# Performance work log

Hardware: AMD Instinct MI355X
Metric: run time of the kernel (lower is better)

Reference implementation:

```python
import jax, jax.numpy as jnp
import numpy as np
from jax.ops import segment_sum, segment_max

IN_CH, HID, OUT_CH, HEADS = 128, 64, 32, 4
N_NODES, N_EDGES = 50000, 800000
NEG_SLOPE = 0.2
EPS = 1e-16


def gat_layer(x, edge_index, W, att_src, att_dst, bias, heads, out_ch, concat):
    """PyG-style GATConv (add_self_loops=False, dropout=0, no edge features)."""
    N = x.shape[0]
    src, dst = edge_index[0], edge_index[1]
    h = (x @ W).reshape(N, heads, out_ch)                 # [N, H, C]
    a_src = jnp.einsum('nhc,hc->nh', h, att_src)          # [N, H]
    a_dst = jnp.einsum('nhc,hc->nh', h, att_dst)          # [N, H]
    e = jax.nn.leaky_relu(a_src[src] + a_dst[dst], NEG_SLOPE)  # [E, H]
    # segment softmax over incoming edges of each dst node
    m = segment_max(e, dst, num_segments=N)               # [N, H]
    ex = jnp.exp(e - m[dst])                              # [E, H]
    s = segment_sum(ex, dst, num_segments=N)              # [N, H]
    alpha = ex / (s[dst] + EPS)                           # [E, H]
    msg = h[src] * alpha[..., None]                       # [E, H, C]
    out = segment_sum(msg, dst, num_segments=N)           # [N, H, C]
    if concat:
        out = out.reshape(N, heads * out_ch)
    else:
        out = out.mean(axis=1)
    return out + bias, alpha


def setup_inputs() -> dict:
    key = jax.random.key(0)
    ks = jax.random.split(key, 10)
    s_in = 1.0 / np.sqrt(IN_CH)
    s_h = 1.0 / np.sqrt(HEADS * HID)
    return {
        'x': jax.random.normal(ks[0], (N_NODES, IN_CH), jnp.float32),
        'edge_index': jax.random.randint(ks[1], (2, N_EDGES), 0, N_NODES, jnp.int32),
        'W1': jax.random.normal(ks[2], (IN_CH, HEADS * HID), jnp.float32) * s_in,
        'att_src1': jax.random.normal(ks[3], (HEADS, HID), jnp.float32) * s_h,
        'att_dst1': jax.random.normal(ks[4], (HEADS, HID), jnp.float32) * s_h,
        'bias1': jnp.zeros((HEADS * HID,), jnp.float32),
        'W2': jax.random.normal(ks[5], (HEADS * HID, OUT_CH), jnp.float32) * s_h,
        'att_src2': jax.random.normal(ks[6], (1, OUT_CH), jnp.float32) * s_h,
        'att_dst2': jax.random.normal(ks[7], (1, OUT_CH), jnp.float32) * s_h,
        'bias2': jnp.zeros((OUT_CH,), jnp.float32),
    }


def reference(x, edge_index, W1, att_src1, att_dst1, bias1, W2, att_src2, att_dst2, bias2):
    h1, alpha1 = gat_layer(x, edge_index, W1, att_src1, att_dst1, bias1, HEADS, HID, concat=True)
    h1 = jax.nn.elu(h1)
    h2, alpha2 = gat_layer(h1, edge_index, W2, att_src2, att_dst2, bias2, 1, OUT_CH, concat=False)
    return h2, edge_index, alpha1, edge_index, alpha2
```

## Files before the change

### kernel.cpp

```cpp
#include <hip/hip_runtime.h>
#include <hip/hip_fp16.h>
#include <math.h>

#define NEG_SLOPE 0.2f
#define EPS_C 1e-16f

typedef _Float16 f16x8 __attribute__((ext_vector_type(8)));
typedef float f32x4 __attribute__((ext_vector_type(4)));

__device__ __forceinline__ float lrelu(float x){ return x > 0.f ? x : NEG_SLOPE * x; }
__device__ __forceinline__ float eluf(float x){ return x > 0.f ? x : expm1f(x); }

__global__ void zero_int_kernel(int* __restrict__ p, int n){
  int i = blockIdx.x * blockDim.x + threadIdx.x;
  if (i < n) p[i] = 0;
}

__global__ void count_deg_kernel(const int* __restrict__ dst, int* __restrict__ deg, int E){
  int i = blockIdx.x * blockDim.x + threadIdx.x;
  if (i < E) atomicAdd(&deg[dst[i]], 1);
}

__global__ __launch_bounds__(256) void scan1_kernel(const int* __restrict__ deg,
    int* __restrict__ offsets, int* __restrict__ blockSums, int N){
  __shared__ int sm[256];
  int b = blockIdx.x, t = threadIdx.x;
  int i = b * 256 + t;
  int v = (i < N) ? deg[i] : 0;
  sm[t] = v;
  __syncthreads();
  #pragma unroll
  for (int st = 1; st < 256; st <<= 1){
    int add = (t >= st) ? sm[t - st] : 0;
    __syncthreads();
    sm[t] += add;
    __syncthreads();
  }
  if (i < N) offsets[i] = sm[t] - v;
  if (t == 255) blockSums[b] = sm[255];
}

__global__ __launch_bounds__(256) void scan2_kernel(const int* __restrict__ blockSums,
    int* __restrict__ blockBase, int* __restrict__ offsetsN, int nb){
  __shared__ int sm[256];
  int t = threadIdx.x;
  int v = (t < nb) ? blockSums[t] : 0;
  sm[t] = v;
  __syncthreads();
  #pragma unroll
  for (int st = 1; st < 256; st <<= 1){
    int add = (t >= st) ? sm[t - st] : 0;
    __syncthreads();
    sm[t] += add;
    __syncthreads();
  }
  if (t < nb) blockBase[t] = sm[t] - v;
  if (t == 255) *offsetsN = sm[255];
}

__global__ __launch_bounds__(256) void scan3_kernel(int* __restrict__ offsets,
    const int* __restrict__ blockBase, int* __restrict__ cursor, int N){
  int b = blockIdx.x, t = threadIdx.x;
  int i = b * 256 + t;
  if (i < N){
    int v = offsets[i] + blockBase[b];
    offsets[i] = v;
    cursor[i] = v;
  }
}

__global__ void scatter_kernel(const int* __restrict__ src, const int* __restrict__ dst,
                               int* __restrict__ cursor, int* __restrict__ csr_src,
                               int* __restrict__ csr_eid, int E){
  int i = blockIdx.x * blockDim.x + threadIdx.x;
  if (i < E){
    int d = dst[i];
    int p = atomicAdd(&cursor[d], 1);
    csr_src[p] = src[i];
    csr_eid[p] = i;
  }
}

__global__ void cvt_x_kernel(const float* __restrict__ x, __half* __restrict__ x16, int n4){
  int i = blockIdx.x * blockDim.x + threadIdx.x;
  if (i < n4){
    float4 v = *reinterpret_cast<const float4*>(&x[(size_t)i * 4]);
    __half2 h01 = __floats2half2_rn(v.x, v.y);
    __half2 h23 = __floats2half2_rn(v.z, v.w);
    uint2 pack;
    pack.x = *reinterpret_cast<unsigned int*>(&h01);
    pack.y = *reinterpret_cast<unsigned int*>(&h23);
    *reinterpret_cast<uint2*>(&x16[(size_t)i * 4]) = pack;
  }
}

__global__ void cvt_w1_kernel(const float* __restrict__ W1, __half* __restrict__ W1t){
  int i = blockIdx.x * blockDim.x + threadIdx.x;
  int k = i >> 8, c = i & 255;
  if (i < 128 * 256) W1t[(size_t)c * 128 + k] = __float2half(W1[(size_t)k * 256 + c]);
}

__global__ void cvt_w2_kernel(const float* __restrict__ W2, __half* __restrict__ W2t){
  int i = blockIdx.x * blockDim.x + threadIdx.x;
  int k = i >> 5, c = i & 31;
  if (i < 256 * 32) W2t[(size_t)c * 256 + k] = __float2half(W2[(size_t)k * 32 + c]);
}

__global__ __launch_bounds__(256) void gemm1_kernel(const __half* __restrict__ x16,
    const __half* __restrict__ W1t, const float* __restrict__ att_src,
    const float* __restrict__ att_dst, __half* __restrict__ h1,
    float* __restrict__ a_src_f, float* __restrict__ a_dst_f, int N){
  __shared__ _Float16 As[128 * 136];
  __shared__ _Float16 Bs[64 * 136];
  int tid = threadIdx.x;
  int lane = tid & 63, wid = tid >> 6;
  int rowBase = blockIdx.x * 128;
  int head = blockIdx.y;
  int colBase = head * 64;

  #pragma unroll
  for (int it = 0; it < 8; ++it){
    int li = it * 256 + tid;
    int r = li >> 4, seg = li & 15;
    int grow = rowBase + r;
    f16x8 v = {};
    if (grow < N) v = *reinterpret_cast<const f16x8*>(&x16[(size_t)grow * 128 + seg * 8]);
    *reinterpret_cast<f16x8*>(&As[r * 136 + seg * 8]) = v;
  }
  #pragma unroll
  for (int it = 0; it < 4; ++it){
    int li = it * 256 + tid;
    int c = li >> 4, seg = li & 15;
    f16x8 v = *reinterpret_cast<const f16x8*>(&W1t[(size_t)(colBase + c) * 128 + seg * 8]);
    *reinterpret_cast<f16x8*>(&Bs[c * 136 + seg * 8]) = v;
  }
  __syncthreads();

  f32x4 acc[2][4] = {};
  int l15 = lane & 15, l4 = lane >> 4;
  #pragma unroll
  for (int ks = 0; ks < 4; ++ks){
    int kOff = ks * 32 + l4 * 8;
    f16x8 a0 = *reinterpret_cast<const f16x8*>(&As[(wid * 32 + l15) * 136 + kOff]);
    f16x8 a1 = *reinterpret_cast<const f16x8*>(&As[(wid * 32 + 16 + l15) * 136 + kOff]);
    #pragma unroll
    for (int cc = 0; cc < 4; ++cc){
      f16x8 b = *reinterpret_cast<const f16x8*>(&Bs[(cc * 16 + l15) * 136 + kOff]);
      acc[0][cc] = __builtin_amdgcn_mfma_f32_16x16x32_f16(a0, b, acc[0][cc], 0, 0, 0);
      acc[1][cc] = __builtin_amdgcn_mfma_f32_16x16x32_f16(a1, b, acc[1][cc], 0, 0, 0);
    }
  }

  #pragma unroll
  for (int rr = 0; rr < 2; ++rr){
    #pragma unroll
    for (int i = 0; i < 4; ++i){
      int row = rowBase + wid * 32 + rr * 16 + l4 * 4 + i;
      if (row < N){
        #pragma unroll
        for (int cc = 0; cc < 4; ++cc)
          h1[(size_t)row * 256 + colBase + cc * 16 + l15] = __float2half(acc[rr][cc][i]);
      }
    }
  }
  float sw[4], dw[4];
  #pragma unroll
  for (int cc = 0; cc < 4; ++cc){
    sw[cc] = att_src[colBase + cc * 16 + l15];
    dw[cc] = att_dst[colBase + cc * 16 + l15];
  }
  #pragma unroll
  for (int rr = 0; rr < 2; ++rr){
    #pragma unroll
    for (int i = 0; i < 4; ++i){
      float ts = 0.f, td = 0.f;
      #pragma unroll
      for (int cc = 0; cc < 4; ++cc){
        ts += acc[rr][cc][i] * sw[cc];
        td += acc[rr][cc][i] * dw[cc];
      }
      #pragma unroll
      for (int st = 8; st > 0; st >>= 1){
        ts += __shfl_xor(ts, st);
        td += __shfl_xor(td, st);
      }
      int row = rowBase + wid * 32 + rr * 16 + l4 * 4 + i;
      if (l15 == 0 && row < N){
        a_src_f[(size_t)row * 4 + head] = ts;
        a_dst_f[(size_t)row * 4 + head] = td;
      }
    }
  }
}

__global__ __launch_bounds__(256) void node1_kernel(
    const __half* __restrict__ h1, const float4* __restrict__ a_src,
    const float* __restrict__ a_src_f, const float4* __restrict__ a_dst,
    const int* __restrict__ offsets, const int* __restrict__ csr_src,
    const int* __restrict__ csr_eid, const float* __restrict__ bias,
    __half* __restrict__ h1b, float* __restrict__ alpha1_out, int N){
  __shared__ float al_lds[4][4][64];
  int gid = blockIdx.x * blockDim.x + threadIdx.x;
  int n = gid >> 6, lane = gid & 63, wid = (threadIdx.x >> 6) & 3;
  if (n >= N) return;
  int off = offsets[n];
  int deg = offsets[n + 1] - off;
  float4 ad = a_dst[n];
  bool have0 = (lane < deg);
  float4 e0 = make_float4(-INFINITY, -INFINITY, -INFINITY, -INFINITY);
  if (have0){
    float4 as = a_src[csr_src[off + lane]];
    e0 = make_float4(lrelu(as.x + ad.x), lrelu(as.y + ad.y),
                     lrelu(as.z + ad.z), lrelu(as.w + ad.w));
  }
  float m0 = e0.x, m1 = e0.y, m2 = e0.z, m3 = e0.w;
  for (int i = lane + 64; i < deg; i += 64){
    float4 as = a_src[csr_src[off + i]];
    m0 = fmaxf(m0, lrelu(as.x + ad.x));
    m1 = fmaxf(m1, lrelu(as.y + ad.y));
    m2 = fmaxf(m2, lrelu(as.z + ad.z));
    m3 = fmaxf(m3, lrelu(as.w + ad.w));
  }
  #pragma unroll
  for (int st = 32; st > 0; st >>= 1){
    m0 = fmaxf(m0, __shfl_xor(m0, st));
    m1 = fmaxf(m1, __shfl_xor(m1, st));
    m2 = fmaxf(m2, __shfl_xor(m2, st));
    m3 = fmaxf(m3, __shfl_xor(m3, st));
  }
  float s0 = 0.f, s1 = 0.f, s2 = 0.f, s3 = 0.f;
  if (have0){
    s0 = __expf(e0.x - m0); s1 = __expf(e0.y - m1);
    s2 = __expf(e0.z - m2); s3 = __expf(e0.w - m3);
  }
  for (int i = lane + 64; i < deg; i += 64){
    float4 as = a_src[csr_src[off + i]];
    s0 += __expf(lrelu(as.x + ad.x) - m0);
    s1 += __expf(lrelu(as.y + ad.y) - m1);
    s2 += __expf(lrelu(as.z + ad.z) - m2);
    s3 += __expf(lrelu(as.w + ad.w) - m3);
  }
  #pragma unroll
  for (int st = 32; st > 0; st >>= 1){
    s0 += __shfl_xor(s0, st); s1 += __shfl_xor(s1, st);
    s2 += __shfl_xor(s2, st); s3 += __shfl_xor(s3, st);
  }
  float i0 = 1.f / (s0 + EPS_C), i1 = 1.f / (s1 + EPS_C);
  float i2 = 1.f / (s2 + EPS_C), i3 = 1.f / (s3 + EPS_C);
  if (have0){
    float a0 = __expf(e0.x - m0) * i0, a1 = __expf(e0.y - m1) * i1;
    float a2 = __expf(e0.z - m2) * i2, a3 = __expf(e0.w - m3) * i3;
    al_lds[wid][0][lane] = a0; al_lds[wid][1][lane] = a1;
    al_lds[wid][2][lane] = a2; al_lds[wid][3][lane] = a3;
    int eid = csr_eid[off + lane];
    *reinterpret_cast<float4*>(&alpha1_out[(size_t)eid * 4]) = make_float4(a0, a1, a2, a3);
  }
  for (int i = lane + 64; i < deg; i += 64){
    int slot = off + i;
    float4 as = a_src[csr_src[slot]];
    int eid = csr_eid[slot];
    *reinterpret_cast<float4*>(&alpha1_out[(size_t)eid * 4]) =
        make_float4(__expf(lrelu(as.x + ad.x) - m0) * i0,
                    __expf(lrelu(as.y + ad.y) - m1) * i1,
                    __expf(lrelu(as.z + ad.z) - m2) * i2,
                    __expf(lrelu(as.w + ad.w) - m3) * i3);
  }
  int head = lane >> 4;
  float mh  = head == 0 ? m0 : head == 1 ? m1 : head == 2 ? m2 : m3;
  float ih  = head == 0 ? i0 : head == 1 ? i1 : head == 2 ? i2 : i3;
  float adh = head == 0 ? ad.x : head == 1 ? ad.y : head == 2 ? ad.z : ad.w;
  float4 accA = make_float4(0.f, 0.f, 0.f, 0.f);
  float4 accB = make_float4(0.f, 0.f, 0.f, 0.f);
  float4 accC = make_float4(0.f, 0.f, 0.f, 0.f);
  float4 accD = make_float4(0.f, 0.f, 0.f, 0.f);
  int degL = deg < 64 ? deg : 64;
  int j = 0;
  for (; j + 3 < degL; j += 4){
    int sA = csr_src[off + j];
    int sB = csr_src[off + j + 1];
    int sC = csr_src[off + j + 2];
    int sD = csr_src[off + j + 3];
    float alA = al_lds[wid][head][j];
    float alB = al_lds[wid][head][j + 1];
    float alC = al_lds[wid][head][j + 2];
    float alD = al_lds[wid][head][j + 3];
    float2 rA = *reinterpret_cast<const float2*>(&h1[(size_t)sA * 256 + lane * 4]);
    float2 rB = *reinterpret_cast<const float2*>(&h1[(size_t)sB * 256 + lane * 4]);
    float2 rC = *reinterpret_cast<const float2*>(&h1[(size_t)sC * 256 + lane * 4]);
    float2 rD = *reinterpret_cast<const float2*>(&h1[(size_t)sD * 256 + lane * 4]);
    float2 fA0 = __half22float2(*reinterpret_cast<__half2*>(&rA.x));
    float2 fA1 = __half22float2(*reinterpret_cast<__half2*>(&rA.y));
    float2 fB0 = __half22float2(*reinterpret_cast<__half2*>(&rB.x));
    float2 fB1 = __half22float2(*reinterpret_cast<__half2*>(&rB.y));
    float2 fC0 = __half22float2(*reinterpret_cast<__half2*>(&rC.x));
    float2 fC1 = __half22float2(*reinterpret_cast<__half2*>(&rC.y));
    float2 fD0 = __half22float2(*reinterpret_cast<__half2*>(&rD.x));
    float2 fD1 = __half22float2(*reinterpret_cast<__half2*>(&rD.y));
    accA.x += alA * fA0.x; accA.y += alA * fA0.y; accA.z += alA * fA1.x; accA.w += alA * fA1.y;
    accB.x += alB * fB0.x; accB.y += alB * fB0.y; accB.z += alB * fB1.x; accB.w += alB * fB1.y;
    accC.x += alC * fC0.x; accC.y += alC * fC0.y; accC.z += alC * fC1.x; accC.w += alC * fC1.y;
    accD.x += alD * fD0.x; accD.y += alD * fD0.y; accD.z += alD * fD1.x; accD.w += alD * fD1.y;
  }
  for (; j < degL; ++j){
    int sA = csr_src[off + j];
    float alA = al_lds[wid][head][j];
    float2 rA = *reinterpret_cast<const float2*>(&h1[(size_t)sA * 256 + lane * 4]);
    float2 fA0 = __half22float2(*reinterpret_cast<__half2*>(&rA.x));
    float2 fA1 = __half22float2(*reinterpret_cast<__half2*>(&rA.y));
    accA.x += alA * fA0.x; accA.y += alA * fA0.y; accA.z += alA * fA1.x; accA.w += alA * fA1.y;
  }
  for (; j < deg; ++j){
    int sA = csr_src[off + j];
    float alA = __expf(lrelu(a_src_f[(size_t)sA * 4 + head] + adh) - mh) * ih;
    float2 rA = *reinterpret_cast<const float2*>(&h1[(size_t)sA * 256 + lane * 4]);
    float2 fA0 = __half22float2(*reinterpret_cast<__half2*>(&rA.x));
    float2 fA1 = __half22float2(*reinterpret_cast<__half2*>(&rA.y));
    accA.x += alA * fA0.x; accA.y += alA * fA0.y; accA.z += alA * fA1.x; accA.w += alA * fA1.y;
  }
  accA.x += accB.x + accC.x + accD.x;
  accA.y += accB.y + accC.y + accD.y;
  accA.z += accB.z + accC.z + accD.z;
  accA.w += accB.w + accC.w + accD.w;
  float4 b = *reinterpret_cast<const float4*>(&bias[lane * 4]);
  __half2 o01 = __floats2half2_rn(eluf(accA.x + b.x), eluf(accA.y + b.y));
  __half2 o23 = __floats2half2_rn(eluf(accA.z + b.z), eluf(accA.w + b.w));
  uint2 pack;
  pack.x = *reinterpret_cast<unsigned int*>(&o01);
  pack.y = *reinterpret_cast<unsigned int*>(&o23);
  *reinterpret_cast<uint2*>(&h1b[(size_t)n * 256 + lane * 4]) = pack;
}

__global__ __launch_bounds__(256) void gemm2_kernel(const __half* __restrict__ h1b,
    const __half* __restrict__ W2t, const float* __restrict__ att_src2,
    const float* __restrict__ att_dst2, __half* __restrict__ h2pre,
    float* __restrict__ a_src2, float* __restrict__ a_dst2, int N){
  __shared__ _Float16 As[128 * 136];
  __shared__ _Float16 Bs[32 * 136];
  int tid = threadIdx.x;
  int lane = tid & 63, wid = tid >> 6;
  int rowBase = blockIdx.x * 128;
  int l15 = lane & 15, l4 = lane >> 4;
  f32x4 acc[2][2] = {};

  for (int kc = 0; kc < 2; ++kc){
    if (kc) __syncthreads();
    #pragma unroll
    for (int it = 0; it < 8; ++it){
      int li = it * 256 + tid;
      int r = li >> 4, seg = li & 15;
      int grow = rowBase + r;
      f16x8 v = {};
      if (grow < N) v = *reinterpret_cast<const f16x8*>(&h1b[(size_t)grow * 256 + kc * 128 + seg * 8]);
      *reinterpret_cast<f16x8*>(&As[r * 136 + seg * 8]) = v;
    }
    #pragma unroll
    for (int it = 0; it < 2; ++it){
      int li = it * 256 + tid;
      int c = li >> 4, seg = li & 15;
      f16x8 v = *reinterpret_cast<const f16x8*>(&W2t[(size_t)c * 256 + kc * 128 + seg * 8]);
      *reinterpret_cast<f16x8*>(&Bs[c * 136 + seg * 8]) = v;
    }
    __syncthreads();
    #pragma unroll
    for (int ks = 0; ks < 4; ++ks){
      int kOff = ks * 32 + l4 * 8;
      f16x8 a0 = *reinterpret_cast<const f16x8*>(&As[(wid * 32 + l15) * 136 + kOff]);
      f16x8 a1 = *reinterpret_cast<const f16x8*>(&As[(wid * 32 + 16 + l15) * 136 + kOff]);
      #pragma unroll
      for (int cb = 0; cb < 2; ++cb){
        f16x8 b = *reinterpret_cast<const f16x8*>(&Bs[(cb * 16 + l15) * 136 + kOff]);
        acc[0][cb] = __builtin_amdgcn_mfma_f32_16x16x32_f16(a0, b, acc[0][cb], 0, 0, 0);
        acc[1][cb] = __builtin_amdgcn_mfma_f32_16x16x32_f16(a1, b, acc[1][cb], 0, 0, 0);
      }
    }
  }
  #pragma unroll
  for (int rr = 0; rr < 2; ++rr){
    #pragma unroll
    for (int i = 0; i < 4; ++i){
      int row = rowBase + wid * 32 + rr * 16 + l4 * 4 + i;
      if (row < N){
        #pragma unroll
        for (int cb = 0; cb < 2; ++cb)
          h2pre[(size_t)row * 32 + cb * 16 + l15] = __float2half(acc[rr][cb][i]);
      }
    }
  }
  float sw0 = att_src2[l15], sw1 = att_src2[16 + l15];
  float dw0 = att_dst2[l15], dw1 = att_dst2[16 + l15];
  #pragma unroll
  for (int rr = 0; rr < 2; ++rr){
    #pragma unroll
    for (int i = 0; i < 4; ++i){
      float ts = acc[rr][0][i] * sw0 + acc[rr][1][i] * sw1;
      float td = acc[rr][0][i] * dw0 + acc[rr][1][i] * dw1;
      #pragma unroll
      for (int st = 8; st > 0; st >>= 1){
        ts += __shfl_xor(ts, st);
        td += __shfl_xor(td, st);
      }
      int row = rowBase + wid * 32 + rr * 16 + l4 * 4 + i;
      if (l15 == 0 && row < N){
        a_src2[row] = ts;
        a_dst2[row] = td;
      }
    }
  }
}

__global__ __launch_bounds__(256) void node2_kernel(
    const __half* __restrict__ h2pre, const float* __restrict__ a_src2,
    const float* __restrict__ a_dst2, const int* __restrict__ offsets,
    const int* __restrict__ csr_src, const int* __restrict__ csr_eid,
    const float* __restrict__ bias2, float* __restrict__ out_h2,
    float* __restrict__ alpha2_out, int N){
  __shared__ float al_lds[4][64];
  int gid = blockIdx.x * blockDim.x + threadIdx.x;
  int n = gid >> 6, lane = gid & 63, wid = (threadIdx.x >> 6) & 3;
  if (n >= N) return;
  int off = offsets[n], deg = offsets[n + 1] - off;
  float adn = a_dst2[n];
  bool have0 = (lane < deg);
  float e0 = -INFINITY;
  if (have0) e0 = lrelu(a_src2[csr_src[off + lane]] + adn);
  float m = e0;
  for (int i = lane + 64; i < deg; i += 64)
    m = fmaxf(m, lrelu(a_src2[csr_src[off + i]] + adn));
  #pragma unroll
  for (int st = 32; st > 0; st >>= 1) m = fmaxf(m, __shfl_xor(m, st));
  float s = have0 ? __expf(e0 - m) : 0.f;
  for (int i = lane + 64; i < deg; i += 64)
    s += __expf(lrelu(a_src2[csr_src[off + i]] + adn) - m);
  #pragma unroll
  for (int st = 32; st > 0; st >>= 1) s += __shfl_xor(s, st);
  float inv = 1.f / (s + EPS_C);
  if (have0){
    float al = __expf(e0 - m) * inv;
    al_lds[wid][lane] = al;
    alpha2_out[csr_eid[off + lane]] = al;
  }
  for (int i = lane + 64; i < deg; i += 64){
    int slot = off + i;
    alpha2_out[csr_eid[slot]] = __expf(lrelu(a_src2[csr_src[slot]] + adn) - m) * inv;
  }
  int c = lane & 31, half = lane >> 5;
  int degL = deg < 64 ? deg : 64;
  float acc = 0.f;
  int j = half;
  for (; j < degL; j += 2){
    int src = csr_src[off + j];
    acc += al_lds[wid][j] * __half2float(h2pre[(size_t)src * 32 + c]);
  }
  for (; j < deg; j += 2){
    int src = csr_src[off + j];
    float al = __expf(lrelu(a_src2[src] + adn) - m) * inv;
    acc += al * __half2float(h2pre[(size_t)src * 32 + c]);
  }
  acc += __shfl_xor(acc, 32);
  if (lane < 32) out_h2[(size_t)n * 32 + c] = acc + bias2[c];
}

__global__ void edge_out_kernel(const int* __restrict__ ei, float* __restrict__ out1,
                                float* __restrict__ out3, int n2e){
  int i = blockIdx.x * blockDim.x + threadIdx.x;
  if (i < n2e){
    float v = (float)ei[i];
    out1[i] = v; out3[i] = v;
  }
}

extern "C" void kernel_launch(void* const* d_in, const int* in_sizes, int n_in,
                              void* d_out, int out_size, void* d_ws, size_t ws_size,
                              hipStream_t stream){
  const float* x        = (const float*)d_in[0];
  const int*   ei       = (const int*)d_in[1];
  const float* W1       = (const float*)d_in[2];
  const float* att_src1 = (const float*)d_in[3];
  const float* att_dst1 = (const float*)d_in[4];
  const float* bias1    = (const float*)d_in[5];
  const float* W2       = (const float*)d_in[6];
  const float* att_src2 = (const float*)d_in[7];
  const float* att_dst2 = (const float*)d_in[8];
  const float* bias2    = (const float*)d_in[9];
  float* out = (float*)d_out;
  (void)n_in; (void)out_size; (void)ws_size;

  const int N = in_sizes[0] / 128;
  const int E = in_sizes[1] / 2;
  const int* src = ei;
  const int* dst = ei + E;
  const int nb = (N + 255) / 256;

  char* ws = (char*)d_ws;
  size_t o = 0;
  auto alloc = [&](size_t bytes) -> void* {
    void* p = ws + o;
    o += (bytes + 255) & ~(size_t)255;
    return p;
  };
  __half* h1      = (__half*)alloc((size_t)N * 256 * 2);
  __half* x16     = (__half*)alloc((size_t)N * 128 * 2);
  __half* W1t     = (__half*)alloc((size_t)256 * 128 * 2);
  __half* W2t     = (__half*)alloc((size_t)32 * 256 * 2);
  __half* h1b     = (__half*)alloc((size_t)N * 256 * 2);
  __half* h2pre   = (__half*)alloc((size_t)N * 32 * 2);
  float*  a_src1  = (float*)alloc((size_t)N * 16);
  float*  a_dst1  = (float*)alloc((size_t)N * 16);
  float*  a_src2  = (float*)alloc((size_t)N * 4);
  float*  a_dst2  = (float*)alloc((size_t)N * 4);
  int*    deg     = (int*)alloc((size_t)N * 4);
  int*    offsets = (int*)alloc((size_t)(N + 1) * 4);
  int*    cursor  = (int*)alloc((size_t)N * 4);
  int*    csr_src = (int*)alloc((size_t)E * 4);
  int*    csr_eid = (int*)alloc((size_t)E * 4);
  int*    blockSums = (int*)alloc(256 * 4);
  int*    blockBase = (int*)alloc(256 * 4);

  const size_t OFF1 = (size_t)N * 32;
  const size_t OFF2 = OFF1 + (size_t)2 * E;
  const size_t OFF3 = OFF2 + (size_t)E * 4;
  const size_t OFF4 = OFF3 + (size_t)2 * E;

  int n4 = (N * 128) / 4;
  hipLaunchKernelGGL(cvt_x_kernel, dim3((n4 + 255) / 256), dim3(256), 0, stream, x, x16, n4);
  hipLaunchKernelGGL(cvt_w1_kernel, dim3(128), dim3(256), 0, stream, W1, W1t);
  hipLaunchKernelGGL(cvt_w2_kernel, dim3(32), dim3(256), 0, stream, W2, W2t);
  hipLaunchKernelGGL(zero_int_kernel, dim3((N + 255) / 256), dim3(256), 0, stream, deg, N);
  hipLaunchKernelGGL(count_deg_kernel, dim3((E + 255) / 256), dim3(256), 0, stream, dst, deg, E);
  hipLaunchKernelGGL(scan1_kernel, dim3(nb), dim3(256), 0, stream, deg, offsets, blockSums, N);
  hipLaunchKernelGGL(scan2_kernel, dim3(1), dim3(256), 0, stream, blockSums, blockBase,
                     offsets + N, nb);
  hipLaunchKernelGGL(scan3_kernel, dim3(nb), dim3(256), 0, stream, offsets, blockBase, cursor, N);
  hipLaunchKernelGGL(scatter_kernel, dim3((E + 255) / 256), dim3(256), 0, stream,
                     src, dst, cursor, csr_src, csr_eid, E);
  hipLaunchKernelGGL(gemm1_kernel, dim3((N + 127) / 128, 4), dim3(256), 0, stream,
                     x16, W1t, att_src1, att_dst1, h1, a_src1, a_dst1, N);
  hipLaunchKernelGGL(node1_kernel, dim3((N * 64 + 255) / 256), dim3(256), 0, stream,
                     h1, (const float4*)a_src1, (const float*)a_src1, (const float4*)a_dst1,
                     offsets, csr_src, csr_eid, bias1, h1b, out + OFF2, N);
  hipLaunchKernelGGL(gemm2_kernel, dim3((N + 127) / 128), dim3(256), 0, stream,
                     h1b, W2t, att_src2, att_dst2, h2pre, a_src2, a_dst2, N);
  hipLaunchKernelGGL(node2_kernel, dim3((N * 64 + 255) / 256), dim3(256), 0, stream,
                     h2pre, a_src2, a_dst2, offsets, csr_src, csr_eid, bias2,
                     out, out + OFF4, N);
  hipLaunchKernelGGL(edge_out_kernel, dim3((2 * E + 255) / 256), dim3(256), 0, stream,
                     ei, out + OFF1, out + OFF3, 2 * E);
}
```

Before: 361.4 us.

## Fuse prep kernels, merge degree count with edge output, deepen gather unroll

Merges the x/W1/W2 conversions and degree zeroing into a single prep kernel. Folds the degree atomic count into the edge_index-to-float output kernel, which removes one pass over dst and two launches. Widens the neighbor gather unroll in node1 from 4 to 8 and adds 4-way independent accumulators in node2, putting more loads in flight. The wider unroll raises register pressure, which can lower occupancy.

```diff
diff --git a/kernel.cpp b/kernel.cpp
--- a/kernel.cpp
+++ b/kernel.cpp
@@ -11,14 +11,47 @@
 __device__ __forceinline__ float lrelu(float x){ return x > 0.f ? x : NEG_SLOPE * x; }
 __device__ __forceinline__ float eluf(float x){ return x > 0.f ? x : expm1f(x); }
 
-__global__ void zero_int_kernel(int* __restrict__ p, int n){
+__global__ void prep_kernel(const float* __restrict__ x, __half* __restrict__ x16,
+                            const float* __restrict__ W1, __half* __restrict__ W1t,
+                            const float* __restrict__ W2, __half* __restrict__ W2t,
+                            int* __restrict__ deg, int n4, int N){
   int i = blockIdx.x * blockDim.x + threadIdx.x;
-  if (i < n) p[i] = 0;
-}
-
-__global__ void count_deg_kernel(const int* __restrict__ dst, int* __restrict__ deg, int E){
+  if (i < n4){
+    float4 v = *reinterpret_cast<const float4*>(&x[(size_t)i * 4]);
+    __half2 h01 = __floats2half2_rn(v.x, v.y);
+    __half2 h23 = __floats2half2_rn(v.z, v.w);
+    uint2 pack;
+    pack.x = *reinterpret_cast<unsigned int*>(&h01);
+    pack.y = *reinterpret_cast<unsigned int*>(&h23);
+    *reinterpret_cast<uint2*>(&x16[(size_t)i * 4]) = pack;
+    return;
+  }
+  int j = i - n4;
+  if (j < 128 * 256){
+    int k = j >> 8, c = j & 255;
+    W1t[(size_t)c * 128 + k] = __float2half(W1[(size_t)k * 256 + c]);
+    return;
+  }
+  j -= 128 * 256;
+  if (j < 256 * 32){
+    int k = j >> 5, c = j & 31;
+    W2t[(size_t)c * 256 + k] = __float2half(W2[(size_t)k * 32 + c]);
+    return;
+  }
+  j -= 256 * 32;
+  if (j < N) deg[j] = 0;
+}
+
+__global__ void edge_deg_kernel(const int* __restrict__ ei, float* __restrict__ out1,
+                                float* __restrict__ out3, int* __restrict__ deg,
+                                int E, int n2e){
   int i = blockIdx.x * blockDim.x + threadIdx.x;
-  if (i < E) atomicAdd(&deg[dst[i]], 1);
+  if (i < n2e){
+    int v = ei[i];
+    float f = (float)v;
+    out1[i] = f; out3[i] = f;
+    if (i >= E) atomicAdd(&deg[v], 1);
+  }
 }
 
 __global__ __launch_bounds__(256) void scan1_kernel(const int* __restrict__ deg,
@@ -79,31 +112,6 @@
     csr_src[p] = src[i];
     csr_eid[p] = i;
   }
-}
-
-__global__ void cvt_x_kernel(const float* __restrict__ x, __half* __restrict__ x16, int n4){
-  int i = blockIdx.x * blockDim.x + threadIdx.x;
-  if (i < n4){
-    float4 v = *reinterpret_cast<const float4*>(&x[(size_t)i * 4]);
-    __half2 h01 = __floats2half2_rn(v.x, v.y);
-    __half2 h23 = __floats2half2_rn(v.z, v.w);
-    uint2 pack;
-    pack.x = *reinterpret_cast<unsigned int*>(&h01);
-    pack.y = *reinterpret_cast<unsigned int*>(&h23);
-    *reinterpret_cast<uint2*>(&x16[(size_t)i * 4]) = pack;
-  }
-}
-
-__global__ void cvt_w1_kernel(const float* __restrict__ W1, __half* __restrict__ W1t){
-  int i = blockIdx.x * blockDim.x + threadIdx.x;
-  int k = i >> 8, c = i & 255;
-  if (i < 128 * 256) W1t[(size_t)c * 128 + k] = __float2half(W1[(size_t)k * 256 + c]);
-}
-
-__global__ void cvt_w2_kernel(const float* __restrict__ W2, __half* __restrict__ W2t){
-  int i = blockIdx.x * blockDim.x + threadIdx.x;
-  int k = i >> 5, c = i & 31;
-  if (i < 256 * 32) W2t[(size_t)c * 256 + k] = __float2half(W2[(size_t)k * 32 + c]);
 }
 
 __global__ __launch_bounds__(256) void gemm1_kernel(const __half* __restrict__ x16,
@@ -269,61 +277,54 @@
   float mh  = head == 0 ? m0 : head == 1 ? m1 : head == 2 ? m2 : m3;
   float ih  = head == 0 ? i0 : head == 1 ? i1 : head == 2 ? i2 : i3;
   float adh = head == 0 ? ad.x : head == 1 ? ad.y : head == 2 ? ad.z : ad.w;
-  float4 accA = make_float4(0.f, 0.f, 0.f, 0.f);
-  float4 accB = make_float4(0.f, 0.f, 0.f, 0.f);
-  float4 accC = make_float4(0.f, 0.f, 0.f, 0.f);
-  float4 accD = make_float4(0.f, 0.f, 0.f, 0.f);
+  float4 acc[8];
+  #pragma unroll
+  for (int u = 0; u < 8; ++u) acc[u] = make_float4(0.f, 0.f, 0.f, 0.f);
   int degL = deg < 64 ? deg : 64;
   int j = 0;
-  for (; j + 3 < degL; j += 4){
-    int sA = csr_src[off + j];
-    int sB = csr_src[off + j + 1];
-    int sC = csr_src[off + j + 2];
-    int sD = csr_src[off + j + 3];
-    float alA = al_lds[wid][head][j];
-    float alB = al_lds[wid][head][j + 1];
-    float alC = al_lds[wid][head][j + 2];
-    float alD = al_lds[wid][head][j + 3];
-    float2 rA = *reinterpret_cast<const float2*>(&h1[(size_t)sA * 256 + lane * 4]);
-    float2 rB = *reinterpret_cast<const float2*>(&h1[(size_t)sB * 256 + lane * 4]);
-    float2 rC = *reinterpret_cast<const float2*>(&h1[(size_t)sC * 256 + lane * 4]);
-    float2 rD = *reinterpret_cast<const float2*>(&h1[(size_t)sD * 256 + lane * 4]);
-    float2 fA0 = __half22float2(*reinterpret_cast<__half2*>(&rA.x));
-    float2 fA1 = __half22float2(*reinterpret_cast<__half2*>(&rA.y));
-    float2 fB0 = __half22float2(*reinterpret_cast<__half2*>(&rB.x));
-    float2 fB1 = __half22float2(*reinterpret_cast<__half2*>(&rB.y));
-    float2 fC0 = __half22float2(*reinterpret_cast<__half2*>(&rC.x));
-    float2 fC1 = __half22float2(*reinterpret_cast<__half2*>(&rC.y));
-    float2 fD0 = __half22float2(*reinterpret_cast<__half2*>(&rD.x));
-    float2 fD1 = __half22float2(*reinterpret_cast<__half2*>(&rD.y));
-    accA.x += alA * fA0.x; accA.y += alA * fA0.y; accA.z += alA * fA1.x; accA.w += alA * fA1.y;
-    accB.x += alB * fB0.x; accB.y += alB * fB0.y; accB.z += alB * fB1.x; accB.w += alB * fB1.y;
-    accC.x += alC * fC0.x; accC.y += alC * fC0.y; accC.z += alC * fC1.x; accC.w += alC * fC1.y;
-    accD.x += alD * fD0.x; accD.y += alD * fD0.y; accD.z += alD * fD1.x; accD.w += alD * fD1.y;
+  for (; j + 7 < degL; j += 8){
+    int s[8];
+    #pragma unroll
+    for (int u = 0; u < 8; ++u) s[u] = csr_src[off + j + u];
+    float2 r[8];
+    #pragma unroll
+    for (int u = 0; u < 8; ++u)
+      r[u] = *reinterpret_cast<const float2*>(&h1[(size_t)s[u] * 256 + lane * 4]);
+    #pragma unroll
+    for (int u = 0; u < 8; ++u){
+      float al = al_lds[wid][head][j + u];
+      float2 f0 = __half22float2(*reinterpret_cast<__half2*>(&r[u].x));
+      float2 f1 = __half22float2(*reinterpret_cast<__half2*>(&r[u].y));
+      acc[u].x += al * f0.x; acc[u].y += al * f0.y;
+      acc[u].z += al * f1.x; acc[u].w += al * f1.y;
+    }
   }
   for (; j < degL; ++j){
     int sA = csr_src[off + j];
-    float alA = al_lds[wid][head][j];
+    float al = al_lds[wid][head][j];
     float2 rA = *reinterpret_cast<const float2*>(&h1[(size_t)sA * 256 + lane * 4]);
-    float2 fA0 = __half22float2(*reinterpret_cast<__half2*>(&rA.x));
-    float2 fA1 = __half22float2(*reinterpret_cast<__half2*>(&rA.y));
-    accA.x += alA * fA0.x; accA.y += alA * fA0.y; accA.z += alA * fA1.x; accA.w += alA * fA1.y;
+    float2 f0 = __half22float2(*reinterpret_cast<__half2*>(&rA.x));
+    float2 f1 = __half22float2(*reinterpret_cast<__half2*>(&rA.y));
+    acc[0].x += al * f0.x; acc[0].y += al * f0.y;
+    acc[0].z += al * f1.x; acc[0].w += al * f1.y;
   }
   for (; j < deg; ++j){
     int sA = csr_src[off + j];
-    float alA = __expf(lrelu(a_src_f[(size_t)sA * 4 + head] + adh) - mh) * ih;
+    float al = __expf(lrelu(a_src_f[(size_t)sA * 4 + head] + adh) - mh) * ih;
     float2 rA = *reinterpret_cast<const float2*>(&h1[(size_t)sA * 256 + lane * 4]);
-    float2 fA0 = __half22float2(*reinterpret_cast<__half2*>(&rA.x));
-    float2 fA1 = __half22float2(*reinterpret_cast<__half2*>(&rA.y));
-    accA.x += alA * fA0.x; accA.y += alA * fA0.y; accA.z += alA * fA1.x; accA.w += alA * fA1.y;
-  }
-  accA.x += accB.x + accC.x + accD.x;
-  accA.y += accB.y + accC.y + accD.y;
-  accA.z += accB.z + accC.z + accD.z;
-  accA.w += accB.w + accC.w + accD.w;
+    float2 f0 = __half22float2(*reinterpret_cast<__half2*>(&rA.x));
+    float2 f1 = __half22float2(*reinterpret_cast<__half2*>(&rA.y));
+    acc[0].x += al * f0.x; acc[0].y += al * f0.y;
+    acc[0].z += al * f1.x; acc[0].w += al * f1.y;
+  }
+  #pragma unroll
+  for (int u = 1; u < 8; ++u){
+    acc[0].x += acc[u].x; acc[0].y += acc[u].y;
+    acc[0].z += acc[u].z; acc[0].w += acc[u].w;
+  }
   float4 b = *reinterpret_cast<const float4*>(&bias[lane * 4]);
-  __half2 o01 = __floats2half2_rn(eluf(accA.x + b.x), eluf(accA.y + b.y));
-  __half2 o23 = __floats2half2_rn(eluf(accA.z + b.z), eluf(accA.w + b.w));
+  __half2 o01 = __floats2half2_rn(eluf(acc[0].x + b.x), eluf(acc[0].y + b.y));
+  __half2 o23 = __floats2half2_rn(eluf(acc[0].z + b.z), eluf(acc[0].w + b.w));
   uint2 pack;
   pack.x = *reinterpret_cast<unsigned int*>(&o01);
   pack.y = *reinterpret_cast<unsigned int*>(&o23);
@@ -445,28 +446,34 @@
   }
   int c = lane & 31, half = lane >> 5;
   int degL = deg < 64 ? deg : 64;
-  float acc = 0.f;
+  float a0 = 0.f, a1 = 0.f, a2 = 0.f, a3 = 0.f;
   int j = half;
+  for (; j + 6 < degL; j += 8){
+    int s0i = csr_src[off + j];
+    int s1i = csr_src[off + j + 2];
+    int s2i = csr_src[off + j + 4];
+    int s3i = csr_src[off + j + 6];
+    float h0 = __half2float(h2pre[(size_t)s0i * 32 + c]);
+    float h1v = __half2float(h2pre[(size_t)s1i * 32 + c]);
+    float h2v = __half2float(h2pre[(size_t)s2i * 32 + c]);
+    float h3v = __half2float(h2pre[(size_t)s3i * 32 + c]);
+    a0 += al_lds[wid][j] * h0;
+    a1 += al_lds[wid][j + 2] * h1v;
+    a2 += al_lds[wid][j + 4] * h2v;
+    a3 += al_lds[wid][j + 6] * h3v;
+  }
   for (; j < degL; j += 2){
     int src = csr_src[off + j];
-    acc += al_lds[wid][j] * __half2float(h2pre[(size_t)src * 32 + c]);
+    a0 += al_lds[wid][j] * __half2float(h2pre[(size_t)src * 32 + c]);
   }
   for (; j < deg; j += 2){
     int src = csr_src[off + j];
     float al = __expf(lrelu(a_src2[src] + adn) - m) * inv;
-    acc += al * __half2float(h2pre[(size_t)src * 32 + c]);
-  }
+    a0 += al * __half2float(h2pre[(size_t)src * 32 + c]);
+  }
+  float acc = a0 + a1 + a2 + a3;
   acc += __shfl_xor(acc, 32);
   if (lane < 32) out_h2[(size_t)n * 32 + c] = acc + bias2[c];
-}
-
-__global__ void edge_out_kernel(const int* __restrict__ ei, float* __restrict__ out1,
-                                float* __restrict__ out3, int n2e){
-  int i = blockIdx.x * blockDim.x + threadIdx.x;
-  if (i < n2e){
-    float v = (float)ei[i];
-    out1[i] = v; out3[i] = v;
-  }
 }
 
 extern "C" void kernel_launch(void* const* d_in, const int* in_sizes, int n_in,
@@ -522,11 +529,11 @@
   const size_t OFF4 = OFF3 + (size_t)2 * E;
 
   int n4 = (N * 128) / 4;
-  hipLaunchKernelGGL(cvt_x_kernel, dim3((n4 + 255) / 256), dim3(256), 0, stream, x, x16, n4);
-  hipLaunchKernelGGL(cvt_w1_kernel, dim3(128), dim3(256), 0, stream, W1, W1t);
-  hipLaunchKernelGGL(cvt_w2_kernel, dim3(32), dim3(256), 0, stream, W2, W2t);
-  hipLaunchKernelGGL(zero_int_kernel, dim3((N + 255) / 256), dim3(256), 0, stream, deg, N);
-  hipLaunchKernelGGL(count_deg_kernel, dim3((E + 255) / 256), dim3(256), 0, stream, dst, deg, E);
+  int prepTotal = n4 + 128 * 256 + 256 * 32 + N;
+  hipLaunchKernelGGL(prep_kernel, dim3((prepTotal + 255) / 256), dim3(256), 0, stream,
+                     x, x16, W1, W1t, W2, W2t, deg, n4, N);
+  hipLaunchKernelGGL(edge_deg_kernel, dim3((2 * E + 255) / 256), dim3(256), 0, stream,
+                     ei, out + OFF1, out + OFF3, deg, E, 2 * E);
   hipLaunchKernelGGL(scan1_kernel, dim3(nb), dim3(256), 0, stream, deg, offsets, blockSums, N);
   hipLaunchKernelGGL(scan2_kernel, dim3(1), dim3(256), 0, stream, blockSums, blockBase,
                      offsets + N, nb);
@@ -543,6 +550,4 @@
   hipLaunchKernelGGL(node2_kernel, dim3((N * 64 + 255) / 256), dim3(256), 0, stream,
                      h2pre, a_src2, a_dst2, offsets, csr_src, csr_eid, bias2,
                      out, out + OFF4, N);
-  hipLaunchKernelGGL(edge_out_kernel, dim3((2 * E + 255) / 256), dim3(256), 0, stream,
-                     ei, out + OFF1, out + OFF3, 2 * E);
-}
+}
```

Measured after the change: 348.6 us. 1.04x faster.
